# Kernel tuning notes

Hardware: AMD Instinct MI355X
Metric: run time of the kernel (lower is better)

The kernel has to match this reference:

```python
import jax, jax.numpy as jnp
import numpy as np

H = 128  # hidden_dim
F = 64   # node_feat_dim


def setup_inputs() -> dict:
    key = jax.random.key(0)
    ks = jax.random.split(key, 24)
    N, E, NR, NT = 50000, 400000, 20000, 20000
    inp = {
        "mol_x": jax.random.normal(ks[0], (N, F), jnp.float32),
        "pos": jax.random.normal(ks[1], (N, 3), jnp.float32),
        "reaction_x": jax.random.normal(ks[2], (NR, F), jnp.float32),
        "target_x": jax.random.normal(ks[3], (NT, F), jnp.float32),
        "edge_index": jax.random.randint(ks[4], (2, E), 0, N, jnp.int32),
    }
    def lin(k, fan_in, fan_out):
        s = 1.0 / np.sqrt(fan_in)
        kw, kb = jax.random.split(k)
        W = jax.random.uniform(kw, (fan_in, fan_out), jnp.float32, -s, s)
        b = jax.random.uniform(kb, (fan_out,), jnp.float32, -s, s)
        return W, b
    inp["W_node"], inp["b_node"] = lin(ks[5], F, H)
    inp["W_att1"], inp["b_att1"] = lin(ks[6], 2 * H + 3, H)
    inp["W_att2"], inp["b_att2"] = lin(ks[7], H, 1)
    inp["W_upd"], inp["b_upd"] = lin(ks[8], H, H)
    inp["Wy1"], inp["by1"] = lin(ks[9], H, 64)
    inp["Wy2"], inp["by2"] = lin(ks[10], 64, 1)
    inp["Wa1"], inp["ba1"] = lin(ks[11], H, 64)
    inp["Wa2"], inp["ba2"] = lin(ks[12], 64, 1)
    return inp


def reference(mol_x, pos, reaction_x, target_x, edge_index,
              W_node, b_node, W_att1, b_att1, W_att2, b_att2,
              W_upd, b_upd, Wy1, by1, Wy2, by2, Wa1, ba1, Wa2, ba2):
    N = mol_x.shape[0]
    # node encoder
    h = mol_x @ W_node + b_node                      # [N, H]
    src, dst = edge_index[0], edge_index[1]          # PyG: x_j = source, x_i = target
    x_j = h[src]                                      # [E, H]
    x_i = h[dst]                                      # [E, H]
    dist = pos[dst] - pos[src]                        # [E, 3]
    cat = jnp.concatenate([x_i, x_j, dist], axis=1)   # [E, 2H+3]
    s = jax.nn.relu(cat @ W_att1 + b_att1) @ W_att2 + b_att2  # [E, 1]
    att = jax.nn.softmax(s, axis=0)                   # global softmax over edges (dim=0)
    msg = x_j * att                                   # [E, H]
    aggr = jax.ops.segment_sum(msg, dst, num_segments=N)  # scatter-add -> [N, H]
    mol_feats = aggr @ W_upd + b_upd                  # [N, H]
    # heads on reaction / target graphs
    rh = reaction_x @ W_node + b_node
    th = target_x @ W_node + b_node
    pred_yield = (jax.nn.relu(rh @ Wy1 + by1) @ Wy2 + by2).squeeze(-1)
    pred_activity = (jax.nn.relu(th @ Wa1 + ba1) @ Wa2 + ba2).squeeze(-1)
    return pred_yield, pred_activity, mol_feats
```

## Files before the change

### kernel.cpp

```cpp
#include <hip/hip_runtime.h>
#include <hip/hip_bf16.h>

typedef unsigned short ushort_t;
typedef __attribute__((ext_vector_type(8))) short s16x8;
typedef __attribute__((ext_vector_type(4))) float f32x4;

__device__ inline unsigned short f2bf(float x) {
    unsigned u = __float_as_uint(x);
    return (unsigned short)((u + 0x7FFFu + ((u >> 16) & 1u)) >> 16);
}
__device__ inline float bflo(unsigned u) { return __uint_as_float(u << 16); }
__device__ inline float bfhi(unsigned u) { return __uint_as_float(u & 0xffff0000u); }

__device__ inline void pack_one(const float* __restrict__ W, int K, int N,
                                ushort_t* __restrict__ dst, int g) {
    int KT = K / 32;
    int nt = g / (KT * 64);
    int rem = g % (KT * 64);
    int kt = rem / 64, lane = rem % 64;
    int n = nt * 16 + (lane & 15);
    int kbase = kt * 32 + ((lane >> 4) << 3);
    ushort_t tmp[8];
#pragma unroll
    for (int j = 0; j < 8; ++j) tmp[j] = f2bf(W[(size_t)(kbase + j) * N + n]);
    uint4 pk;
    pk.x = tmp[0] | ((unsigned)tmp[1] << 16);
    pk.y = tmp[2] | ((unsigned)tmp[3] << 16);
    pk.z = tmp[4] | ((unsigned)tmp[5] << 16);
    pk.w = tmp[6] | ((unsigned)tmp[7] << 16);
    *(uint4*)&dst[(size_t)g * 8] = pk;
}

__global__ void convert_w(const float* __restrict__ Wn, const float* __restrict__ W1,
                          const float* __restrict__ Wu, const float* __restrict__ Wy1,
                          const float* __restrict__ Wa1,
                          ushort_t* __restrict__ Wnb, ushort_t* __restrict__ W1tb,
                          ushort_t* __restrict__ W1mb, ushort_t* __restrict__ Wub,
                          ushort_t* __restrict__ Wy1b, ushort_t* __restrict__ Wa1b,
                          int* __restrict__ counts, int N) {
    int t = blockIdx.x * 256 + threadIdx.x;
    if (t < 1024)       pack_one(Wn, 64, 128, Wnb, t);
    else if (t < 3072)  pack_one(W1, 128, 128, W1tb, t - 1024);
    else if (t < 5120)  pack_one(W1 + 128 * 128, 128, 128, W1mb, t - 3072);
    else if (t < 7168)  pack_one(Wu, 128, 128, Wub, t - 5120);
    else if (t < 8192)  pack_one(Wy1, 128, 64, Wy1b, t - 7168);
    else if (t < 9216)  pack_one(Wa1, 128, 64, Wa1b, t - 8192);
    if (t < N) counts[t] = 0;
}

__global__ void encode_pq(const float* __restrict__ x, const ushort_t* __restrict__ Wnb,
                          const float* __restrict__ bn, const ushort_t* __restrict__ W1tb,
                          const ushort_t* __restrict__ W1mb, const float* __restrict__ b1,
                          ushort_t* __restrict__ hb, ushort_t* __restrict__ P,
                          ushort_t* __restrict__ Q, const int* __restrict__ dst,
                          int* __restrict__ counts, int nrows, int E) {
    __shared__ ushort_t ldsH[4 * 16 * 136];
    int t = threadIdx.x;
    for (int e = blockIdx.x * 256 + t; e < E; e += gridDim.x * 256)
        atomicAdd(&counts[dst[e]], 1);
    int w = t >> 6, lane = t & 63;
    int c = lane & 15, q = lane >> 4;
    int r0 = blockIdx.x * 64 + w * 16;
    int rowA = r0 + c; if (rowA >= nrows) rowA = nrows - 1;
    ushort_t* myH = &ldsH[w * 16 * 136];

    s16x8 xa[2];
#pragma unroll
    for (int kt = 0; kt < 2; ++kt) {
        const float* xp = &x[(size_t)rowA * 64 + kt * 32 + q * 8];
        float4 v0 = *(const float4*)xp;
        float4 v1 = *(const float4*)(xp + 4);
        s16x8 a;
        a[0] = (short)f2bf(v0.x); a[1] = (short)f2bf(v0.y);
        a[2] = (short)f2bf(v0.z); a[3] = (short)f2bf(v0.w);
        a[4] = (short)f2bf(v1.x); a[5] = (short)f2bf(v1.y);
        a[6] = (short)f2bf(v1.z); a[7] = (short)f2bf(v1.w);
        xa[kt] = a;
    }
#pragma unroll
    for (int nt = 0; nt < 8; ++nt) {
        f32x4 acc = {0.f, 0.f, 0.f, 0.f};
#pragma unroll
        for (int kt = 0; kt < 2; ++kt) {
            s16x8 b = *(const s16x8*)&Wnb[((nt * 2 + kt) * 64 + lane) * 8];
            acc = __builtin_amdgcn_mfma_f32_16x16x32_bf16(xa[kt], b, acc, 0, 0, 0);
        }
        float bi = bn[nt * 16 + c];
#pragma unroll
        for (int r = 0; r < 4; ++r) {
            int row = r0 + q * 4 + r;
            ushort_t hv = f2bf(acc[r] + bi);
            myH[(q * 4 + r) * 136 + nt * 16 + c] = hv;
            if (row < nrows) hb[(size_t)row * 128 + nt * 16 + c] = hv;
        }
    }
    __syncthreads();
    s16x8 ha[4];
#pragma unroll
    for (int kt = 0; kt < 4; ++kt)
        ha[kt] = *(const s16x8*)&myH[c * 136 + kt * 32 + q * 8];
#pragma unroll
    for (int nt = 0; nt < 8; ++nt) {
        f32x4 pa = {0.f, 0.f, 0.f, 0.f}, qa = pa;
#pragma unroll
        for (int kt = 0; kt < 4; ++kt) {
            s16x8 bp = *(const s16x8*)&W1tb[((nt * 4 + kt) * 64 + lane) * 8];
            s16x8 bq = *(const s16x8*)&W1mb[((nt * 4 + kt) * 64 + lane) * 8];
            pa = __builtin_amdgcn_mfma_f32_16x16x32_bf16(ha[kt], bp, pa, 0, 0, 0);
            qa = __builtin_amdgcn_mfma_f32_16x16x32_bf16(ha[kt], bq, qa, 0, 0, 0);
        }
        float bi = b1[nt * 16 + c];
#pragma unroll
        for (int r = 0; r < 4; ++r) {
            int row = r0 + q * 4 + r;
            if (row < nrows) {
                P[(size_t)row * 128 + nt * 16 + c] = f2bf(pa[r] + bi);
                Q[(size_t)row * 128 + nt * 16 + c] = f2bf(qa[r]);
            }
        }
    }
}

__global__ void scan1(const int* __restrict__ counts, int* __restrict__ offs,
                      int* __restrict__ partials, int N) {
    __shared__ int sm[256];
    int i = blockIdx.x * 256 + threadIdx.x;
    int v = (i < N) ? counts[i] : 0;
    sm[threadIdx.x] = v; __syncthreads();
    for (int off = 1; off < 256; off <<= 1) {
        int add = (threadIdx.x >= off) ? sm[threadIdx.x - off] : 0;
        __syncthreads();
        sm[threadIdx.x] += add;
        __syncthreads();
    }
    if (i < N) offs[i] = sm[threadIdx.x] - v;
    if (threadIdx.x == 255) partials[blockIdx.x] = sm[255];
}

__global__ void scan_add(int* __restrict__ offs, int* __restrict__ cursor,
                         const int* __restrict__ partials, int nb, int N) {
    __shared__ int sm[256];
    int t = threadIdx.x;
    sm[t] = (t < nb && t < blockIdx.x) ? partials[t] : 0;
    __syncthreads();
    for (int off = 128; off > 0; off >>= 1) {
        if (t < off) sm[t] += sm[t + off];
        __syncthreads();
    }
    int basev = sm[0];
    int i = blockIdx.x * 256 + t;
    if (i < N) {
        int v = offs[i] + basev;
        offs[i] = v;
        cursor[i] = v;
    }
}

__global__ void edge_score(const ushort_t* __restrict__ P, const ushort_t* __restrict__ Q,
                           const float* __restrict__ pos, const int* __restrict__ src,
                           const int* __restrict__ dst, const float* __restrict__ W1b,
                           const float* __restrict__ W2, const float* __restrict__ b2,
                           int* __restrict__ cursor, int2* __restrict__ csr,
                           float* __restrict__ redm, float* __restrict__ rede, int E) {
    __shared__ float wsh[512];
    __shared__ float smm[256], sme[256];
    int t = threadIdx.x;
    for (int i = t; i < 384; i += 256) wsh[i] = W1b[i];
    if (t < 128) wsh[384 + t] = W2[t];
    __syncthreads();
    int w = t >> 6, lane = t & 63;
    int g = lane >> 4, c = lane & 15;
    float w0[8], w1[8], w2[8], wv[8];
#pragma unroll
    for (int j = 0; j < 8; ++j) {
        w0[j] = wsh[c * 8 + j];
        w1[j] = wsh[128 + c * 8 + j];
        w2[j] = wsh[256 + c * 8 + j];
        wv[j] = wsh[384 + c * 8 + j];
    }
    float b2v = b2[0];
    int base = blockIdx.x * 128 + w * 32;
    float m = -1e30f, ev = 0.f;
#pragma unroll
    for (int it = 0; it < 8; ++it) {
        int e = base + it * 4 + g;
        bool valid = e < E;
        int ee = valid ? e : (E - 1);
        int sa = src[ee], da = dst[ee];
        int p = 0;
        if (c == 0 && valid) p = atomicAdd(&cursor[da], 1);
        uint4 pr = *(const uint4*)&P[(size_t)da * 128 + c * 8];
        uint4 qr = *(const uint4*)&Q[(size_t)sa * 128 + c * 8];
        float d0 = pos[da * 3]     - pos[sa * 3];
        float d1 = pos[da * 3 + 1] - pos[sa * 3 + 1];
        float d2 = pos[da * 3 + 2] - pos[sa * 3 + 2];
        unsigned pw[4] = {pr.x, pr.y, pr.z, pr.w};
        unsigned qw[4] = {qr.x, qr.y, qr.z, qr.w};
        float v = 0.f;
#pragma unroll
        for (int jj = 0; jj < 4; ++jj) {
            float pe = bflo(pw[jj]) + bflo(qw[jj])
                     + d0 * w0[2 * jj] + d1 * w1[2 * jj] + d2 * w2[2 * jj];
            float po = bfhi(pw[jj]) + bfhi(qw[jj])
                     + d0 * w0[2 * jj + 1] + d1 * w1[2 * jj + 1] + d2 * w2[2 * jj + 1];
            v += fmaxf(pe, 0.f) * wv[2 * jj] + fmaxf(po, 0.f) * wv[2 * jj + 1];
        }
#pragma unroll
        for (int off = 1; off < 16; off <<= 1) v += __shfl_xor(v, off, 64);
        if (c == 0 && valid) {
            float sv = v + b2v;
            csr[p] = make_int2(sa, __float_as_int(sv));
            float nm = fmaxf(m, sv);
            ev = ev * __expf(m - nm) + __expf(sv - nm);
            m = nm;
        }
    }
    smm[t] = m; sme[t] = ev; __syncthreads();
    for (int off = 128; off > 0; off >>= 1) {
        if (t < off) {
            float m1 = smm[t], m2 = smm[t + off];
            float e1 = sme[t], e2 = sme[t + off];
            float M = fmaxf(m1, m2);
            smm[t] = M;
            sme[t] = e1 * __expf(m1 - M) + e2 * __expf(m2 - M);
        }
        __syncthreads();
    }
    if (t == 0) { redm[blockIdx.x] = smm[0]; rede[blockIdx.x] = sme[0]; }
}

__global__ void gather_head(const ushort_t* __restrict__ hb, const int2* __restrict__ csr,
                            const int* __restrict__ offs, const int* __restrict__ deg,
                            const float* __restrict__ redm, const float* __restrict__ rede,
                            int nbE,
                            const ushort_t* __restrict__ Wub, const float* __restrict__ bu,
                            float* __restrict__ molf, int N, int nbG,
                            const float* __restrict__ rx, const float* __restrict__ tx,
                            const ushort_t* __restrict__ Wnb, const float* __restrict__ bn,
                            const ushort_t* __restrict__ Wy1b, const float* __restrict__ by1,
                            const float* __restrict__ Wy2, const float* __restrict__ by2,
                            const ushort_t* __restrict__ Wa1b, const float* __restrict__ ba1,
                            const float* __restrict__ Wa2, const float* __restrict__ ba2,
                            float* __restrict__ out, int nb1, int NR, int NT) {
    int t = threadIdx.x;
    int w = t >> 6, lane = t & 63;
    int c = lane & 15, q = lane >> 4;

    if (blockIdx.x < nbG) {
        __shared__ ushort_t ldsA[16 * 136];
        __shared__ float smm[256], sme[256];
        float m = -1e30f, z = 0.f;
        for (int i = t; i < nbE; i += 256) {
            float m2 = redm[i], z2 = rede[i];
            float M = fmaxf(m, m2);
            z = z * __expf(m - M) + z2 * __expf(m2 - M);
            m = M;
        }
        smm[t] = m; sme[t] = z; __syncthreads();
        for (int off = 128; off > 0; off >>= 1) {
            if (t < off) {
                float m1 = smm[t], m2 = smm[t + off];
                float e1 = sme[t], e2 = sme[t + off];
                float M = fmaxf(m1, m2);
                smm[t] = M;
                sme[t] = e1 * __expf(m1 - M) + e2 * __expf(m2 - M);
            }
            __syncthreads();
        }
        float gm = smm[0], inv = 1.f / sme[0];
        __syncthreads();

        int g = lane >> 4;
        int r0 = blockIdx.x * 16;
#pragma unroll
        for (int i = 0; i < 4; ++i) {
            int node = r0 + w * 4 + i;
            float a[8] = {0.f, 0.f, 0.f, 0.f, 0.f, 0.f, 0.f, 0.f};
            if (node < N) {
                int start = offs[node], d = deg[node];
                int k = g;
                for (; k + 4 < d; k += 8) {
                    int2 v0 = csr[start + k];
                    int2 v1 = csr[start + k + 4];
                    uint4 h0 = *(const uint4*)&hb[(size_t)v0.x * 128 + c * 8];
                    uint4 h1 = *(const uint4*)&hb[(size_t)v1.x * 128 + c * 8];
                    float at0 = __expf(__int_as_float(v0.y) - gm) * inv;
                    float at1 = __expf(__int_as_float(v1.y) - gm) * inv;
                    a[0] += bflo(h0.x) * at0; a[1] += bfhi(h0.x) * at0;
                    a[2] += bflo(h0.y) * at0; a[3] += bfhi(h0.y) * at0;
                    a[4] += bflo(h0.z) * at0; a[5] += bfhi(h0.z) * at0;
                    a[6] += bflo(h0.w) * at0; a[7] += bfhi(h0.w) * at0;
                    a[0] += bflo(h1.x) * at1; a[1] += bfhi(h1.x) * at1;
                    a[2] += bflo(h1.y) * at1; a[3] += bfhi(h1.y) * at1;
                    a[4] += bflo(h1.z) * at1; a[5] += bfhi(h1.z) * at1;
                    a[6] += bflo(h1.w) * at1; a[7] += bfhi(h1.w) * at1;
                }
                if (k < d) {
                    int2 v0 = csr[start + k];
                    uint4 h0 = *(const uint4*)&hb[(size_t)v0.x * 128 + c * 8];
                    float at0 = __expf(__int_as_float(v0.y) - gm) * inv;
                    a[0] += bflo(h0.x) * at0; a[1] += bfhi(h0.x) * at0;
                    a[2] += bflo(h0.y) * at0; a[3] += bfhi(h0.y) * at0;
                    a[4] += bflo(h0.z) * at0; a[5] += bfhi(h0.z) * at0;
                    a[6] += bflo(h0.w) * at0; a[7] += bfhi(h0.w) * at0;
                }
            }
#pragma unroll
            for (int j = 0; j < 8; ++j) {
                a[j] += __shfl_xor(a[j], 16, 64);
                a[j] += __shfl_xor(a[j], 32, 64);
            }
            if (g == 0) {
                uint4 pk;
                pk.x = f2bf(a[0]) | ((unsigned)f2bf(a[1]) << 16);
                pk.y = f2bf(a[2]) | ((unsigned)f2bf(a[3]) << 16);
                pk.z = f2bf(a[4]) | ((unsigned)f2bf(a[5]) << 16);
                pk.w = f2bf(a[6]) | ((unsigned)f2bf(a[7]) << 16);
                *(uint4*)&ldsA[(w * 4 + i) * 136 + c * 8] = pk;
            }
        }
        __syncthreads();
        int ntA = w, ntB = w + 4;
        f32x4 acc0 = {0.f, 0.f, 0.f, 0.f}, acc1 = acc0;
#pragma unroll
        for (int kt = 0; kt < 4; ++kt) {
            s16x8 av = *(const s16x8*)&ldsA[c * 136 + kt * 32 + q * 8];
            s16x8 b0 = *(const s16x8*)&Wub[((ntA * 4 + kt) * 64 + lane) * 8];
            s16x8 b1 = *(const s16x8*)&Wub[((ntB * 4 + kt) * 64 + lane) * 8];
            acc0 = __builtin_amdgcn_mfma_f32_16x16x32_bf16(av, b0, acc0, 0, 0, 0);
            acc1 = __builtin_amdgcn_mfma_f32_16x16x32_bf16(av, b1, acc1, 0, 0, 0);
        }
        float bi0 = bu[ntA * 16 + c], bi1 = bu[ntB * 16 + c];
#pragma unroll
        for (int r = 0; r < 4; ++r) {
            int row = r0 + q * 4 + r;
            if (row < N) {
                molf[(size_t)row * 128 + ntA * 16 + c] = acc0[r] + bi0;
                molf[(size_t)row * 128 + ntB * 16 + c] = acc1[r] + bi1;
            }
        }
    } else {
        __shared__ ushort_t ldsX[16 * 72];
        __shared__ ushort_t ldsB[16 * 136];
        __shared__ float part[64];
        int blk = blockIdx.x - nbG;
        const float* x; const ushort_t* W1b; const float* b1; const float* W2; const float* b2;
        float* o; int r0, nrows;
        if (blk < nb1) { x = rx; W1b = Wy1b; b1 = by1; W2 = Wy2; b2 = by2; o = out; r0 = blk * 16; nrows = NR; }
        else { x = tx; W1b = Wa1b; b1 = ba1; W2 = Wa2; b2 = ba2; o = out + NR; r0 = (blk - nb1) * 16; nrows = NT; }
        {
            int row = t >> 4, c4 = (t & 15) * 4;
            float4 v = *(const float4*)&x[(size_t)(r0 + row) * 64 + c4];
            uint2 pk;
            pk.x = f2bf(v.x) | ((unsigned)f2bf(v.y) << 16);
            pk.y = f2bf(v.z) | ((unsigned)f2bf(v.w) << 16);
            *(uint2*)&ldsX[row * 72 + c4] = pk;
        }
        __syncthreads();
        {
            int ntA = w, ntB = w + 4;
            f32x4 acc0 = {0.f, 0.f, 0.f, 0.f}, acc1 = acc0;
#pragma unroll
            for (int kt = 0; kt < 2; ++kt) {
                s16x8 a = *(const s16x8*)&ldsX[c * 72 + kt * 32 + q * 8];
                s16x8 b0 = *(const s16x8*)&Wnb[((ntA * 2 + kt) * 64 + lane) * 8];
                s16x8 b1v = *(const s16x8*)&Wnb[((ntB * 2 + kt) * 64 + lane) * 8];
                acc0 = __builtin_amdgcn_mfma_f32_16x16x32_bf16(a, b0, acc0, 0, 0, 0);
                acc1 = __builtin_amdgcn_mfma_f32_16x16x32_bf16(a, b1v, acc1, 0, 0, 0);
            }
            float bi0 = bn[ntA * 16 + c], bi1 = bn[ntB * 16 + c];
#pragma unroll
            for (int r = 0; r < 4; ++r) {
                int row = q * 4 + r;
                ldsB[row * 136 + ntA * 16 + c] = f2bf(acc0[r] + bi0);
                ldsB[row * 136 + ntB * 16 + c] = f2bf(acc1[r] + bi1);
            }
        }
        __syncthreads();
        {
            f32x4 acc = {0.f, 0.f, 0.f, 0.f};
#pragma unroll
            for (int kt = 0; kt < 4; ++kt) {
                s16x8 a = *(const s16x8*)&ldsB[c * 136 + kt * 32 + q * 8];
                s16x8 b0 = *(const s16x8*)&W1b[((w * 4 + kt) * 64 + lane) * 8];
                acc = __builtin_amdgcn_mfma_f32_16x16x32_bf16(a, b0, acc, 0, 0, 0);
            }
            float bi = b1[w * 16 + c], w2v = W2[w * 16 + c];
#pragma unroll
            for (int r = 0; r < 4; ++r) {
                float u = fmaxf(acc[r] + bi, 0.f) * w2v;
#pragma unroll
                for (int mm = 1; mm < 16; mm <<= 1) u += __shfl_xor(u, mm, 64);
                if (c == 0) part[w * 16 + q * 4 + r] = u;
            }
        }
        __syncthreads();
        if (t < 16) {
            int row = r0 + t;
            if (row < nrows)
                o[row] = part[t] + part[16 + t] + part[32 + t] + part[48 + t] + b2[0];
        }
    }
}

extern "C" void kernel_launch(void* const* d_in, const int* in_sizes, int n_in,
                              void* d_out, int out_size, void* d_ws, size_t ws_size,
                              hipStream_t stream) {
    const float* mol_x      = (const float*)d_in[0];
    const float* pos        = (const float*)d_in[1];
    const float* reaction_x = (const float*)d_in[2];
    const float* target_x   = (const float*)d_in[3];
    const int*   ei         = (const int*)d_in[4];
    const float* W_node = (const float*)d_in[5];
    const float* b_node = (const float*)d_in[6];
    const float* W_att1 = (const float*)d_in[7];
    const float* b_att1 = (const float*)d_in[8];
    const float* W_att2 = (const float*)d_in[9];
    const float* b_att2 = (const float*)d_in[10];
    const float* W_upd  = (const float*)d_in[11];
    const float* b_upd  = (const float*)d_in[12];
    const float* Wy1 = (const float*)d_in[13];
    const float* by1 = (const float*)d_in[14];
    const float* Wy2 = (const float*)d_in[15];
    const float* by2 = (const float*)d_in[16];
    const float* Wa1 = (const float*)d_in[17];
    const float* ba1 = (const float*)d_in[18];
    const float* Wa2 = (const float*)d_in[19];
    const float* ba2 = (const float*)d_in[20];

    int N  = in_sizes[0] / 64;
    int E  = in_sizes[4] / 2;
    int NR = in_sizes[2] / 64;
    int NT = in_sizes[3] / 64;

    float* out = (float*)d_out;

    int nbE = (E + 127) / 128;
    int nbG = (N + 15) / 16;
    int nbH = (NR + NT) / 16;

    char* wp = (char*)d_ws;
    ushort_t* hb = (ushort_t*)wp;  wp += (size_t)N * 128 * 2;
    ushort_t* Qb = (ushort_t*)wp;  wp += (size_t)N * 128 * 2;
    float* redm  = (float*)wp;     wp += (size_t)nbE * 4;
    float* rede  = (float*)wp;     wp += (size_t)nbE * 4;
    int* counts  = (int*)wp;       wp += (size_t)N * 4;
    int* offs    = (int*)wp;       wp += (size_t)N * 4;
    int* cursor  = (int*)wp;       wp += (size_t)N * 4;
    int* partials= (int*)wp;       wp += 256 * 4;
    int2* csr    = (int2*)wp;      wp += (size_t)E * 8;
    ushort_t* Wnb  = (ushort_t*)wp; wp += 8192 * 2;
    ushort_t* W1tb = (ushort_t*)wp; wp += 16384 * 2;
    ushort_t* W1mb = (ushort_t*)wp; wp += 16384 * 2;
    ushort_t* Wub  = (ushort_t*)wp; wp += 16384 * 2;
    ushort_t* Wy1b = (ushort_t*)wp; wp += 8192 * 2;
    ushort_t* Wa1b = (ushort_t*)wp; wp += 8192 * 2;
    ushort_t* Pb = (ushort_t*)(out + NR + NT);
    float* molf  = out + NR + NT;

    const int* srcp = ei;
    const int* dstp = ei + E;
    int nbN = (N + 255) / 256;

    convert_w<<<nbN, 256, 0, stream>>>(W_node, W_att1, W_upd, Wy1, Wa1,
                                       Wnb, W1tb, W1mb, Wub, Wy1b, Wa1b, counts, N);
    encode_pq<<<(N + 63) / 64, 256, 0, stream>>>(mol_x, Wnb, b_node, W1tb, W1mb, b_att1,
                                                 hb, Pb, Qb, dstp, counts, N, E);
    scan1<<<nbN, 256, 0, stream>>>(counts, offs, partials, N);
    scan_add<<<nbN, 256, 0, stream>>>(offs, cursor, partials, nbN, N);
    edge_score<<<nbE, 256, 0, stream>>>(Pb, Qb, pos, srcp, dstp,
                                        W_att1 + 256 * 128, W_att2, b_att2,
                                        cursor, csr, redm, rede, E);
    gather_head<<<nbG + nbH, 256, 0, stream>>>(hb, csr, offs, counts, redm, rede, nbE,
                                               Wub, b_upd, molf, N, nbG,
                                               reaction_x, target_x, Wnb, b_node,
                                               Wy1b, by1, Wy2, by2, Wa1b, ba1, Wa2, ba2,
                                               out, NR / 16, NR, NT);
}
```

Measured before the change: 232.3 us.

## Fuse two-pass scan into one kernel and move head MLPs into edge-score launch

The two-kernel exclusive scan is replaced by a single kernel in which each block re-sums all preceding counts directly, dropping one launch and the partials buffer at the cost of redundant reads of earlier counts (quadratic total work across blocks, about 196 blocks). The reaction/target head blocks move from the gather kernel into the edge-score launch, so they run alongside edge scoring and the gather kernel only does aggregation plus the update GEMM. The intent is fewer launches and better overlap of the independent head work with the memory-bound edge phase.

```diff
diff --git a/kernel.cpp b/kernel.cpp
--- a/kernel.cpp
+++ b/kernel.cpp
@@ -121,101 +121,201 @@
     }
 }
 
-__global__ void scan1(const int* __restrict__ counts, int* __restrict__ offs,
-                      int* __restrict__ partials, int N) {
-    __shared__ int sm[256];
-    int i = blockIdx.x * 256 + threadIdx.x;
-    int v = (i < N) ? counts[i] : 0;
-    sm[threadIdx.x] = v; __syncthreads();
-    for (int off = 1; off < 256; off <<= 1) {
-        int add = (threadIdx.x >= off) ? sm[threadIdx.x - off] : 0;
-        __syncthreads();
-        sm[threadIdx.x] += add;
-        __syncthreads();
-    }
-    if (i < N) offs[i] = sm[threadIdx.x] - v;
-    if (threadIdx.x == 255) partials[blockIdx.x] = sm[255];
-}
-
-__global__ void scan_add(int* __restrict__ offs, int* __restrict__ cursor,
-                         const int* __restrict__ partials, int nb, int N) {
+__global__ void scan_fused(const int* __restrict__ counts, int* __restrict__ offs,
+                           int* __restrict__ cursor, int N) {
     __shared__ int sm[256];
     int t = threadIdx.x;
-    sm[t] = (t < nb && t < blockIdx.x) ? partials[t] : 0;
-    __syncthreads();
+    int limit = blockIdx.x * 256;
+    int acc = 0;
+    for (int i = t; i < limit; i += 256) acc += counts[i];
+    sm[t] = acc; __syncthreads();
     for (int off = 128; off > 0; off >>= 1) {
         if (t < off) sm[t] += sm[t + off];
         __syncthreads();
     }
-    int basev = sm[0];
-    int i = blockIdx.x * 256 + t;
-    if (i < N) {
-        int v = offs[i] + basev;
-        offs[i] = v;
-        cursor[i] = v;
-    }
-}
-
-__global__ void edge_score(const ushort_t* __restrict__ P, const ushort_t* __restrict__ Q,
-                           const float* __restrict__ pos, const int* __restrict__ src,
-                           const int* __restrict__ dst, const float* __restrict__ W1b,
-                           const float* __restrict__ W2, const float* __restrict__ b2,
-                           int* __restrict__ cursor, int2* __restrict__ csr,
-                           float* __restrict__ redm, float* __restrict__ rede, int E) {
-    __shared__ float wsh[512];
+    int base = sm[0];
+    __syncthreads();
+    int idx = limit + t;
+    int v = (idx < N) ? counts[idx] : 0;
+    sm[t] = v; __syncthreads();
+    for (int off = 1; off < 256; off <<= 1) {
+        int add = (t >= off) ? sm[t - off] : 0;
+        __syncthreads();
+        sm[t] += add;
+        __syncthreads();
+    }
+    if (idx < N) {
+        int val = base + sm[t] - v;
+        offs[idx] = val;
+        cursor[idx] = val;
+    }
+}
+
+__global__ void edge_score_heads(const ushort_t* __restrict__ P, const ushort_t* __restrict__ Q,
+                                 const float* __restrict__ pos, const int* __restrict__ src,
+                                 const int* __restrict__ dst, const float* __restrict__ W1b,
+                                 const float* __restrict__ W2, const float* __restrict__ b2,
+                                 int* __restrict__ cursor, int2* __restrict__ csr,
+                                 float* __restrict__ redm, float* __restrict__ rede,
+                                 int E, int nbE,
+                                 const float* __restrict__ rx, const float* __restrict__ tx,
+                                 const ushort_t* __restrict__ Wnb, const float* __restrict__ bn,
+                                 const ushort_t* __restrict__ Wy1b, const float* __restrict__ by1,
+                                 const float* __restrict__ Wy2, const float* __restrict__ by2,
+                                 const ushort_t* __restrict__ Wa1b, const float* __restrict__ ba1,
+                                 const float* __restrict__ Wa2, const float* __restrict__ ba2,
+                                 float* __restrict__ out, int nb1, int NR, int NT) {
+    int t = threadIdx.x;
+    int w = t >> 6, lane = t & 63;
+
+    if (blockIdx.x < nbE) {
+        __shared__ float wsh[512];
+        __shared__ float smm[256], sme[256];
+        for (int i = t; i < 384; i += 256) wsh[i] = W1b[i];
+        if (t < 128) wsh[384 + t] = W2[t];
+        __syncthreads();
+        int g = lane >> 4, c = lane & 15;
+        float w0[8], w1[8], w2[8], wv[8];
+#pragma unroll
+        for (int j = 0; j < 8; ++j) {
+            w0[j] = wsh[c * 8 + j];
+            w1[j] = wsh[128 + c * 8 + j];
+            w2[j] = wsh[256 + c * 8 + j];
+            wv[j] = wsh[384 + c * 8 + j];
+        }
+        float b2v = b2[0];
+        int base = blockIdx.x * 128 + w * 32;
+        float m = -1e30f, ev = 0.f;
+#pragma unroll
+        for (int it = 0; it < 8; ++it) {
+            int e = base + it * 4 + g;
+            bool valid = e < E;
+            int ee = valid ? e : (E - 1);
+            int sa = src[ee], da = dst[ee];
+            int p = 0;
+            if (c == 0 && valid) p = atomicAdd(&cursor[da], 1);
+            uint4 pr = *(const uint4*)&P[(size_t)da * 128 + c * 8];
+            uint4 qr = *(const uint4*)&Q[(size_t)sa * 128 + c * 8];
+            float d0 = pos[da * 3]     - pos[sa * 3];
+            float d1 = pos[da * 3 + 1] - pos[sa * 3 + 1];
+            float d2 = pos[da * 3 + 2] - pos[sa * 3 + 2];
+            unsigned pw[4] = {pr.x, pr.y, pr.z, pr.w};
+            unsigned qw[4] = {qr.x, qr.y, qr.z, qr.w};
+            float v = 0.f;
+#pragma unroll
+            for (int jj = 0; jj < 4; ++jj) {
+                float pe = bflo(pw[jj]) + bflo(qw[jj])
+                         + d0 * w0[2 * jj] + d1 * w1[2 * jj] + d2 * w2[2 * jj];
+                float po = bfhi(pw[jj]) + bfhi(qw[jj])
+                         + d0 * w0[2 * jj + 1] + d1 * w1[2 * jj + 1] + d2 * w2[2 * jj + 1];
+                v += fmaxf(pe, 0.f) * wv[2 * jj] + fmaxf(po, 0.f) * wv[2 * jj + 1];
+            }
+#pragma unroll
+            for (int off = 1; off < 16; off <<= 1) v += __shfl_xor(v, off, 64);
+            if (c == 0 && valid) {
+                float sv = v + b2v;
+                csr[p] = make_int2(sa, __float_as_int(sv));
+                float nm = fmaxf(m, sv);
+                ev = ev * __expf(m - nm) + __expf(sv - nm);
+                m = nm;
+            }
+        }
+        smm[t] = m; sme[t] = ev; __syncthreads();
+        for (int off = 128; off > 0; off >>= 1) {
+            if (t < off) {
+                float m1 = smm[t], m2 = smm[t + off];
+                float e1 = sme[t], e2 = sme[t + off];
+                float M = fmaxf(m1, m2);
+                smm[t] = M;
+                sme[t] = e1 * __expf(m1 - M) + e2 * __expf(m2 - M);
+            }
+            __syncthreads();
+        }
+        if (t == 0) { redm[blockIdx.x] = smm[0]; rede[blockIdx.x] = sme[0]; }
+    } else {
+        __shared__ ushort_t ldsX[16 * 72];
+        __shared__ ushort_t ldsB[16 * 136];
+        __shared__ float part[64];
+        int c = lane & 15, q = lane >> 4;
+        int blk = blockIdx.x - nbE;
+        const float* x; const ushort_t* W1bh; const float* b1; const float* W2h; const float* b2h;
+        float* o; int r0, nrows;
+        if (blk < nb1) { x = rx; W1bh = Wy1b; b1 = by1; W2h = Wy2; b2h = by2; o = out; r0 = blk * 16; nrows = NR; }
+        else { x = tx; W1bh = Wa1b; b1 = ba1; W2h = Wa2; b2h = ba2; o = out + NR; r0 = (blk - nb1) * 16; nrows = NT; }
+        {
+            int row = t >> 4, c4 = (t & 15) * 4;
+            float4 v = *(const float4*)&x[(size_t)(r0 + row) * 64 + c4];
+            uint2 pk;
+            pk.x = f2bf(v.x) | ((unsigned)f2bf(v.y) << 16);
+            pk.y = f2bf(v.z) | ((unsigned)f2bf(v.w) << 16);
+            *(uint2*)&ldsX[row * 72 + c4] = pk;
+        }
+        __syncthreads();
+        {
+            int ntA = w, ntB = w + 4;
+            f32x4 acc0 = {0.f, 0.f, 0.f, 0.f}, acc1 = acc0;
+#pragma unroll
+            for (int kt = 0; kt < 2; ++kt) {
+                s16x8 a = *(const s16x8*)&ldsX[c * 72 + kt * 32 + q * 8];
+                s16x8 b0 = *(const s16x8*)&Wnb[((ntA * 2 + kt) * 64 + lane) * 8];
+                s16x8 b1v = *(const s16x8*)&Wnb[((ntB * 2 + kt) * 64 + lane) * 8];
+                acc0 = __builtin_amdgcn_mfma_f32_16x16x32_bf16(a, b0, acc0, 0, 0, 0);
+                acc1 = __builtin_amdgcn_mfma_f32_16x16x32_bf16(a, b1v, acc1, 0, 0, 0);
+            }
+            float bi0 = bn[ntA * 16 + c], bi1 = bn[ntB * 16 + c];
+#pragma unroll
+            for (int r = 0; r < 4; ++r) {
+                int row = q * 4 + r;
+                ldsB[row * 136 + ntA * 16 + c] = f2bf(acc0[r] + bi0);
+                ldsB[row * 136 + ntB * 16 + c] = f2bf(acc1[r] + bi1);
+            }
+        }
+        __syncthreads();
+        {
+            f32x4 acc = {0.f, 0.f, 0.f, 0.f};
+#pragma unroll
+            for (int kt = 0; kt < 4; ++kt) {
+                s16x8 a = *(const s16x8*)&ldsB[c * 136 + kt * 32 + q * 8];
+                s16x8 b0 = *(const s16x8*)&W1bh[((w * 4 + kt) * 64 + lane) * 8];
+                acc = __builtin_amdgcn_mfma_f32_16x16x32_bf16(a, b0, acc, 0, 0, 0);
+            }
+            float bi = b1[w * 16 + c], w2v = W2h[w * 16 + c];
+#pragma unroll
+            for (int r = 0; r < 4; ++r) {
+                float u = fmaxf(acc[r] + bi, 0.f) * w2v;
+#pragma unroll
+                for (int mm = 1; mm < 16; mm <<= 1) u += __shfl_xor(u, mm, 64);
+                if (c == 0) part[w * 16 + q * 4 + r] = u;
+            }
+        }
+        __syncthreads();
+        if (t < 16) {
+            int row = r0 + t;
+            if (row < nrows)
+                o[row] = part[t] + part[16 + t] + part[32 + t] + part[48 + t] + b2h[0];
+        }
+    }
+}
+
+__global__ void gather_upd(const ushort_t* __restrict__ hb, const int2* __restrict__ csr,
+                           const int* __restrict__ offs, const int* __restrict__ deg,
+                           const float* __restrict__ redm, const float* __restrict__ rede,
+                           int nbE,
+                           const ushort_t* __restrict__ Wub, const float* __restrict__ bu,
+                           float* __restrict__ molf, int N) {
+    __shared__ ushort_t ldsA[16 * 136];
     __shared__ float smm[256], sme[256];
     int t = threadIdx.x;
-    for (int i = t; i < 384; i += 256) wsh[i] = W1b[i];
-    if (t < 128) wsh[384 + t] = W2[t];
-    __syncthreads();
     int w = t >> 6, lane = t & 63;
-    int g = lane >> 4, c = lane & 15;
-    float w0[8], w1[8], w2[8], wv[8];
-#pragma unroll
-    for (int j = 0; j < 8; ++j) {
-        w0[j] = wsh[c * 8 + j];
-        w1[j] = wsh[128 + c * 8 + j];
-        w2[j] = wsh[256 + c * 8 + j];
-        wv[j] = wsh[384 + c * 8 + j];
-    }
-    float b2v = b2[0];
-    int base = blockIdx.x * 128 + w * 32;
-    float m = -1e30f, ev = 0.f;
-#pragma unroll
-    for (int it = 0; it < 8; ++it) {
-        int e = base + it * 4 + g;
-        bool valid = e < E;
-        int ee = valid ? e : (E - 1);
-        int sa = src[ee], da = dst[ee];
-        int p = 0;
-        if (c == 0 && valid) p = atomicAdd(&cursor[da], 1);
-        uint4 pr = *(const uint4*)&P[(size_t)da * 128 + c * 8];
-        uint4 qr = *(const uint4*)&Q[(size_t)sa * 128 + c * 8];
-        float d0 = pos[da * 3]     - pos[sa * 3];
-        float d1 = pos[da * 3 + 1] - pos[sa * 3 + 1];
-        float d2 = pos[da * 3 + 2] - pos[sa * 3 + 2];
-        unsigned pw[4] = {pr.x, pr.y, pr.z, pr.w};
-        unsigned qw[4] = {qr.x, qr.y, qr.z, qr.w};
-        float v = 0.f;
-#pragma unroll
-        for (int jj = 0; jj < 4; ++jj) {
-            float pe = bflo(pw[jj]) + bflo(qw[jj])
-                     + d0 * w0[2 * jj] + d1 * w1[2 * jj] + d2 * w2[2 * jj];
-            float po = bfhi(pw[jj]) + bfhi(qw[jj])
-                     + d0 * w0[2 * jj + 1] + d1 * w1[2 * jj + 1] + d2 * w2[2 * jj + 1];
-            v += fmaxf(pe, 0.f) * wv[2 * jj] + fmaxf(po, 0.f) * wv[2 * jj + 1];
-        }
-#pragma unroll
-        for (int off = 1; off < 16; off <<= 1) v += __shfl_xor(v, off, 64);
-        if (c == 0 && valid) {
-            float sv = v + b2v;
-            csr[p] = make_int2(sa, __float_as_int(sv));
-            float nm = fmaxf(m, sv);
-            ev = ev * __expf(m - nm) + __expf(sv - nm);
-            m = nm;
-        }
-    }
-    smm[t] = m; sme[t] = ev; __syncthreads();
+    int c = lane & 15, q = lane >> 4;
+    float m = -1e30f, z = 0.f;
+    for (int i = t; i < nbE; i += 256) {
+        float m2 = redm[i], z2 = rede[i];
+        float M = fmaxf(m, m2);
+        z = z * __expf(m - M) + z2 * __expf(m2 - M);
+        m = M;
+    }
+    smm[t] = m; sme[t] = z; __syncthreads();
     for (int off = 128; off > 0; off >>= 1) {
         if (t < off) {
             float m1 = smm[t], m2 = smm[t + off];
@@ -226,179 +326,76 @@
         }
         __syncthreads();
     }
-    if (t == 0) { redm[blockIdx.x] = smm[0]; rede[blockIdx.x] = sme[0]; }
-}
-
-__global__ void gather_head(const ushort_t* __restrict__ hb, const int2* __restrict__ csr,
-                            const int* __restrict__ offs, const int* __restrict__ deg,
-                            const float* __restrict__ redm, const float* __restrict__ rede,
-                            int nbE,
-                            const ushort_t* __restrict__ Wub, const float* __restrict__ bu,
-                            float* __restrict__ molf, int N, int nbG,
-                            const float* __restrict__ rx, const float* __restrict__ tx,
-                            const ushort_t* __restrict__ Wnb, const float* __restrict__ bn,
-                            const ushort_t* __restrict__ Wy1b, const float* __restrict__ by1,
-                            const float* __restrict__ Wy2, const float* __restrict__ by2,
-                            const ushort_t* __restrict__ Wa1b, const float* __restrict__ ba1,
-                            const float* __restrict__ Wa2, const float* __restrict__ ba2,
-                            float* __restrict__ out, int nb1, int NR, int NT) {
-    int t = threadIdx.x;
-    int w = t >> 6, lane = t & 63;
-    int c = lane & 15, q = lane >> 4;
-
-    if (blockIdx.x < nbG) {
-        __shared__ ushort_t ldsA[16 * 136];
-        __shared__ float smm[256], sme[256];
-        float m = -1e30f, z = 0.f;
-        for (int i = t; i < nbE; i += 256) {
-            float m2 = redm[i], z2 = rede[i];
-            float M = fmaxf(m, m2);
-            z = z * __expf(m - M) + z2 * __expf(m2 - M);
-            m = M;
-        }
-        smm[t] = m; sme[t] = z; __syncthreads();
-        for (int off = 128; off > 0; off >>= 1) {
-            if (t < off) {
-                float m1 = smm[t], m2 = smm[t + off];
-                float e1 = sme[t], e2 = sme[t + off];
-                float M = fmaxf(m1, m2);
-                smm[t] = M;
-                sme[t] = e1 * __expf(m1 - M) + e2 * __expf(m2 - M);
-            }
-            __syncthreads();
-        }
-        float gm = smm[0], inv = 1.f / sme[0];
-        __syncthreads();
-
-        int g = lane >> 4;
-        int r0 = blockIdx.x * 16;
-#pragma unroll
-        for (int i = 0; i < 4; ++i) {
-            int node = r0 + w * 4 + i;
-            float a[8] = {0.f, 0.f, 0.f, 0.f, 0.f, 0.f, 0.f, 0.f};
-            if (node < N) {
-                int start = offs[node], d = deg[node];
-                int k = g;
-                for (; k + 4 < d; k += 8) {
-                    int2 v0 = csr[start + k];
-                    int2 v1 = csr[start + k + 4];
-                    uint4 h0 = *(const uint4*)&hb[(size_t)v0.x * 128 + c * 8];
-                    uint4 h1 = *(const uint4*)&hb[(size_t)v1.x * 128 + c * 8];
-                    float at0 = __expf(__int_as_float(v0.y) - gm) * inv;
-                    float at1 = __expf(__int_as_float(v1.y) - gm) * inv;
-                    a[0] += bflo(h0.x) * at0; a[1] += bfhi(h0.x) * at0;
-                    a[2] += bflo(h0.y) * at0; a[3] += bfhi(h0.y) * at0;
-                    a[4] += bflo(h0.z) * at0; a[5] += bfhi(h0.z) * at0;
-                    a[6] += bflo(h0.w) * at0; a[7] += bfhi(h0.w) * at0;
-                    a[0] += bflo(h1.x) * at1; a[1] += bfhi(h1.x) * at1;
-                    a[2] += bflo(h1.y) * at1; a[3] += bfhi(h1.y) * at1;
-                    a[4] += bflo(h1.z) * at1; a[5] += bfhi(h1.z) * at1;
-                    a[6] += bflo(h1.w) * at1; a[7] += bfhi(h1.w) * at1;
-                }
-                if (k < d) {
-                    int2 v0 = csr[start + k];
-                    uint4 h0 = *(const uint4*)&hb[(size_t)v0.x * 128 + c * 8];
-                    float at0 = __expf(__int_as_float(v0.y) - gm) * inv;
-                    a[0] += bflo(h0.x) * at0; a[1] += bfhi(h0.x) * at0;
-                    a[2] += bflo(h0.y) * at0; a[3] += bfhi(h0.y) * at0;
-                    a[4] += bflo(h0.z) * at0; a[5] += bfhi(h0.z) * at0;
-                    a[6] += bflo(h0.w) * at0; a[7] += bfhi(h0.w) * at0;
-                }
-            }
-#pragma unroll
-            for (int j = 0; j < 8; ++j) {
-                a[j] += __shfl_xor(a[j], 16, 64);
-                a[j] += __shfl_xor(a[j], 32, 64);
-            }
-            if (g == 0) {
-                uint4 pk;
-                pk.x = f2bf(a[0]) | ((unsigned)f2bf(a[1]) << 16);
-                pk.y = f2bf(a[2]) | ((unsigned)f2bf(a[3]) << 16);
-                pk.z = f2bf(a[4]) | ((unsigned)f2bf(a[5]) << 16);
-                pk.w = f2bf(a[6]) | ((unsigned)f2bf(a[7]) << 16);
-                *(uint4*)&ldsA[(w * 4 + i) * 136 + c * 8] = pk;
-            }
-        }
-        __syncthreads();
-        int ntA = w, ntB = w + 4;
-        f32x4 acc0 = {0.f, 0.f, 0.f, 0.f}, acc1 = acc0;
-#pragma unroll
-        for (int kt = 0; kt < 4; ++kt) {
-            s16x8 av = *(const s16x8*)&ldsA[c * 136 + kt * 32 + q * 8];
-            s16x8 b0 = *(const s16x8*)&Wub[((ntA * 4 + kt) * 64 + lane) * 8];
-            s16x8 b1 = *(const s16x8*)&Wub[((ntB * 4 + kt) * 64 + lane) * 8];
-            acc0 = __builtin_amdgcn_mfma_f32_16x16x32_bf16(av, b0, acc0, 0, 0, 0);
-            acc1 = __builtin_amdgcn_mfma_f32_16x16x32_bf16(av, b1, acc1, 0, 0, 0);
-        }
-        float bi0 = bu[ntA * 16 + c], bi1 = bu[ntB * 16 + c];
-#pragma unroll
-        for (int r = 0; r < 4; ++r) {
-            int row = r0 + q * 4 + r;
-            if (row < N) {
-                molf[(size_t)row * 128 + ntA * 16 + c] = acc0[r] + bi0;
-                molf[(size_t)row * 128 + ntB * 16 + c] = acc1[r] + bi1;
-            }
-        }
-    } else {
-        __shared__ ushort_t ldsX[16 * 72];
-        __shared__ ushort_t ldsB[16 * 136];
-        __shared__ float part[64];
-        int blk = blockIdx.x - nbG;
-        const float* x; const ushort_t* W1b; const float* b1; const float* W2; const float* b2;
-        float* o; int r0, nrows;
-        if (blk < nb1) { x = rx; W1b = Wy1b; b1 = by1; W2 = Wy2; b2 = by2; o = out; r0 = blk * 16; nrows = NR; }
-        else { x = tx; W1b = Wa1b; b1 = ba1; W2 = Wa2; b2 = ba2; o = out + NR; r0 = (blk - nb1) * 16; nrows = NT; }
-        {
-            int row = t >> 4, c4 = (t & 15) * 4;
-            float4 v = *(const float4*)&x[(size_t)(r0 + row) * 64 + c4];
-            uint2 pk;
-            pk.x = f2bf(v.x) | ((unsigned)f2bf(v.y) << 16);
-            pk.y = f2bf(v.z) | ((unsigned)f2bf(v.w) << 16);
-            *(uint2*)&ldsX[row * 72 + c4] = pk;
-        }
-        __syncthreads();
-        {
-            int ntA = w, ntB = w + 4;
-            f32x4 acc0 = {0.f, 0.f, 0.f, 0.f}, acc1 = acc0;
-#pragma unroll
-            for (int kt = 0; kt < 2; ++kt) {
-                s16x8 a = *(const s16x8*)&ldsX[c * 72 + kt * 32 + q * 8];
-                s16x8 b0 = *(const s16x8*)&Wnb[((ntA * 2 + kt) * 64 + lane) * 8];
-                s16x8 b1v = *(const s16x8*)&Wnb[((ntB * 2 + kt) * 64 + lane) * 8];
-                acc0 = __builtin_amdgcn_mfma_f32_16x16x32_bf16(a, b0, acc0, 0, 0, 0);
-                acc1 = __builtin_amdgcn_mfma_f32_16x16x32_bf16(a, b1v, acc1, 0, 0, 0);
-            }
-            float bi0 = bn[ntA * 16 + c], bi1 = bn[ntB * 16 + c];
-#pragma unroll
-            for (int r = 0; r < 4; ++r) {
-                int row = q * 4 + r;
-                ldsB[row * 136 + ntA * 16 + c] = f2bf(acc0[r] + bi0);
-                ldsB[row * 136 + ntB * 16 + c] = f2bf(acc1[r] + bi1);
-            }
-        }
-        __syncthreads();
-        {
-            f32x4 acc = {0.f, 0.f, 0.f, 0.f};
-#pragma unroll
-            for (int kt = 0; kt < 4; ++kt) {
-                s16x8 a = *(const s16x8*)&ldsB[c * 136 + kt * 32 + q * 8];
-                s16x8 b0 = *(const s16x8*)&W1b[((w * 4 + kt) * 64 + lane) * 8];
-                acc = __builtin_amdgcn_mfma_f32_16x16x32_bf16(a, b0, acc, 0, 0, 0);
-            }
-            float bi = b1[w * 16 + c], w2v = W2[w * 16 + c];
-#pragma unroll
-            for (int r = 0; r < 4; ++r) {
-                float u = fmaxf(acc[r] + bi, 0.f) * w2v;
-#pragma unroll
-                for (int mm = 1; mm < 16; mm <<= 1) u += __shfl_xor(u, mm, 64);
-                if (c == 0) part[w * 16 + q * 4 + r] = u;
-            }
-        }
-        __syncthreads();
-        if (t < 16) {
-            int row = r0 + t;
-            if (row < nrows)
-                o[row] = part[t] + part[16 + t] + part[32 + t] + part[48 + t] + b2[0];
+    float gm = smm[0], inv = 1.f / sme[0];
+    __syncthreads();
+
+    int g = lane >> 4;
+    int r0 = blockIdx.x * 16;
+#pragma unroll
+    for (int i = 0; i < 4; ++i) {
+        int node = r0 + w * 4 + i;
+        float a[8] = {0.f, 0.f, 0.f, 0.f, 0.f, 0.f, 0.f, 0.f};
+        if (node < N) {
+            int start = offs[node], d = deg[node];
+            int k = g;
+            for (; k + 4 < d; k += 8) {
+                int2 v0 = csr[start + k];
+                int2 v1 = csr[start + k + 4];
+                uint4 h0 = *(const uint4*)&hb[(size_t)v0.x * 128 + c * 8];
+                uint4 h1 = *(const uint4*)&hb[(size_t)v1.x * 128 + c * 8];
+                float at0 = __expf(__int_as_float(v0.y) - gm) * inv;
+                float at1 = __expf(__int_as_float(v1.y) - gm) * inv;
+                a[0] += bflo(h0.x) * at0; a[1] += bfhi(h0.x) * at0;
+                a[2] += bflo(h0.y) * at0; a[3] += bfhi(h0.y) * at0;
+                a[4] += bflo(h0.z) * at0; a[5] += bfhi(h0.z) * at0;
+                a[6] += bflo(h0.w) * at0; a[7] += bfhi(h0.w) * at0;
+                a[0] += bflo(h1.x) * at1; a[1] += bfhi(h1.x) * at1;
+                a[2] += bflo(h1.y) * at1; a[3] += bfhi(h1.y) * at1;
+                a[4] += bflo(h1.z) * at1; a[5] += bfhi(h1.z) * at1;
+                a[6] += bflo(h1.w) * at1; a[7] += bfhi(h1.w) * at1;
+            }
+            if (k < d) {
+                int2 v0 = csr[start + k];
+                uint4 h0 = *(const uint4*)&hb[(size_t)v0.x * 128 + c * 8];
+                float at0 = __expf(__int_as_float(v0.y) - gm) * inv;
+                a[0] += bflo(h0.x) * at0; a[1] += bfhi(h0.x) * at0;
+                a[2] += bflo(h0.y) * at0; a[3] += bfhi(h0.y) * at0;
+                a[4] += bflo(h0.z) * at0; a[5] += bfhi(h0.z) * at0;
+                a[6] += bflo(h0.w) * at0; a[7] += bfhi(h0.w) * at0;
+            }
+        }
+#pragma unroll
+        for (int j = 0; j < 8; ++j) {
+            a[j] += __shfl_xor(a[j], 16, 64);
+            a[j] += __shfl_xor(a[j], 32, 64);
+        }
+        if (g == 0) {
+            uint4 pk;
+            pk.x = f2bf(a[0]) | ((unsigned)f2bf(a[1]) << 16);
+            pk.y = f2bf(a[2]) | ((unsigned)f2bf(a[3]) << 16);
+            pk.z = f2bf(a[4]) | ((unsigned)f2bf(a[5]) << 16);
+            pk.w = f2bf(a[6]) | ((unsigned)f2bf(a[7]) << 16);
+            *(uint4*)&ldsA[(w * 4 + i) * 136 + c * 8] = pk;
+        }
+    }
+    __syncthreads();
+    int ntA = w, ntB = w + 4;
+    f32x4 acc0 = {0.f, 0.f, 0.f, 0.f}, acc1 = acc0;
+#pragma unroll
+    for (int kt = 0; kt < 4; ++kt) {
+        s16x8 av = *(const s16x8*)&ldsA[c * 136 + kt * 32 + q * 8];
+        s16x8 b0 = *(const s16x8*)&Wub[((ntA * 4 + kt) * 64 + lane) * 8];
+        s16x8 b1 = *(const s16x8*)&Wub[((ntB * 4 + kt) * 64 + lane) * 8];
+        acc0 = __builtin_amdgcn_mfma_f32_16x16x32_bf16(av, b0, acc0, 0, 0, 0);
+        acc1 = __builtin_amdgcn_mfma_f32_16x16x32_bf16(av, b1, acc1, 0, 0, 0);
+    }
+    float bi0 = bu[ntA * 16 + c], bi1 = bu[ntB * 16 + c];
+#pragma unroll
+    for (int r = 0; r < 4; ++r) {
+        int row = r0 + q * 4 + r;
+        if (row < N) {
+            molf[(size_t)row * 128 + ntA * 16 + c] = acc0[r] + bi0;
+            molf[(size_t)row * 128 + ntB * 16 + c] = acc1[r] + bi1;
         }
     }
 }
@@ -447,7 +444,6 @@
     int* counts  = (int*)wp;       wp += (size_t)N * 4;
     int* offs    = (int*)wp;       wp += (size_t)N * 4;
     int* cursor  = (int*)wp;       wp += (size_t)N * 4;
-    int* partials= (int*)wp;       wp += 256 * 4;
     int2* csr    = (int2*)wp;      wp += (size_t)E * 8;
     ushort_t* Wnb  = (ushort_t*)wp; wp += 8192 * 2;
     ushort_t* W1tb = (ushort_t*)wp; wp += 16384 * 2;
@@ -466,14 +462,13 @@
                                        Wnb, W1tb, W1mb, Wub, Wy1b, Wa1b, counts, N);
     encode_pq<<<(N + 63) / 64, 256, 0, stream>>>(mol_x, Wnb, b_node, W1tb, W1mb, b_att1,
                                                  hb, Pb, Qb, dstp, counts, N, E);
-    scan1<<<nbN, 256, 0, stream>>>(counts, offs, partials, N);
-    scan_add<<<nbN, 256, 0, stream>>>(offs, cursor, partials, nbN, N);
-    edge_score<<<nbE, 256, 0, stream>>>(Pb, Qb, pos, srcp, dstp,
-                                        W_att1 + 256 * 128, W_att2, b_att2,
-                                        cursor, csr, redm, rede, E);
-    gather_head<<<nbG + nbH, 256, 0, stream>>>(hb, csr, offs, counts, redm, rede, nbE,
-                                               Wub, b_upd, molf, N, nbG,
-                                               reaction_x, target_x, Wnb, b_node,
-                                               Wy1b, by1, Wy2, by2, Wa1b, ba1, Wa2, ba2,
-                                               out, NR / 16, NR, NT);
-}
+    scan_fused<<<nbN, 256, 0, stream>>>(counts, offs, cursor, N);
+    edge_score_heads<<<nbE + nbH, 256, 0, stream>>>(Pb, Qb, pos, srcp, dstp,
+                                                    W_att1 + 256 * 128, W_att2, b_att2,
+                                                    cursor, csr, redm, rede, E, nbE,
+                                                    reaction_x, target_x, Wnb, b_node,
+                                                    Wy1b, by1, Wy2, by2, Wa1b, ba1, Wa2, ba2,
+                                                    out, NR / 16, NR, NT);
+    gather_upd<<<nbG, 256, 0, stream>>>(hb, csr, offs, counts, redm, rede, nbE,
+                                        Wub, b_upd, molf, N);
+}
```

Result: slower. 252.3 us (+8.6%).
